# Kernel tuning notes

Measured on AMD Instinct MI355X. Metric: run time of the kernel, lower is better.

The kernel has to match this reference:

```python
import jax, jax.numpy as jnp
from jax import lax
import numpy as np

K = 31      # avg_pool2d kernel_size
PAD = 15    # avg_pool2d padding
EPS = 1.0
GAMMA = 5.0


def _box_avg(x):
    # Separable 31x31 box filter, stride 1, zero padding 15,
    # count_include_pad=True (PyTorch default) -> always divide by K*K.
    s = lax.reduce_window(x, 0.0, lax.add, (1, 1, K, 1), (1, 1, 1, 1),
                          [(0, 0), (0, 0), (PAD, PAD), (0, 0)])
    s = lax.reduce_window(s, 0.0, lax.add, (1, 1, 1, K), (1, 1, 1, 1),
                          [(0, 0), (0, 0), (0, 0), (PAD, PAD)])
    return s / (K * K)


def setup_inputs() -> dict:
    key = jax.random.key(0)
    k1, k2 = jax.random.split(key)
    shape = (64, 1, 512, 512)  # [B, C, H, W]
    inp = jax.random.uniform(k1, shape, dtype=jnp.float32)
    tgt = jax.random.uniform(k2, shape, dtype=jnp.float32)
    return {"input": inp, "target": tgt}


def reference(input, target):
    weight = 1.0 + GAMMA * jnp.abs(_box_avg(target) - target)
    intersection = jnp.sum(input * target * weight)
    denom = jnp.sum(input * weight) + jnp.sum(target * weight)
    dice = (2.0 * intersection + EPS) / (denom + EPS)
    return 1.0 - dice
```

## Files before the change

kernel.cpp:

```cpp
#include <hip/hip_runtime.h>


#define BATCH 64
#define H     512
#define W     512
#define PADR  15
#define NSEG  32
#define RB    (H / NSEG)
#define NBLK  (BATCH * NSEG)

__global__ __launch_bounds__(64) void fused_kernel(const float* __restrict__ tgt,
                                                   const float* __restrict__ inp,
                                                   float4* __restrict__ partials) {
    const int lane = threadIdx.x;
    const int blk  = blockIdx.x;
    const int band = blk & (NSEG - 1);
    const int b    = blk >> 5;
    const int r0   = band * RB;
    const int col0 = lane * 8;
    const float* timg = tgt + (size_t)b * H * W;
    const float* iimg = inp + (size_t)b * H * W;

    float vr[8];
    #pragma unroll
    for (int k = 0; k < 8; ++k) vr[k] = 0.f;
    #pragma unroll
    for (int j = -PADR; j <= PADR; ++j) {
        const int r = r0 + j;
        if (r >= 0 && r < H) {
            const float4 a = *(const float4*)(timg + (size_t)r * W + col0);
            const float4 c = *(const float4*)(timg + (size_t)r * W + col0 + 4);
            vr[0] += a.x; vr[1] += a.y; vr[2] += a.z; vr[3] += a.w;
            vr[4] += c.x; vr[5] += c.y; vr[6] += c.z; vr[7] += c.w;
        }
    }

    float validf[40];
    #pragma unroll
    for (int m = 0; m < 40; ++m) {
        const int c = col0 - 16 + m;
        validf[m] = (c >= 0 && c < W) ? 1.f : 0.f;
    }

    const float inv = 1.0f / 961.0f;
    float aI = 0.f, aA = 0.f, aB = 0.f;

    for (int h = r0; h < r0 + RB; ++h) {
        float wd[40];
        #pragma unroll
        for (int k = 0; k < 8; ++k) {
            wd[k]      = __shfl_up(vr[k], 2, 64);
            wd[k + 8]  = __shfl_up(vr[k], 1, 64);
            wd[k + 16] = vr[k];
            wd[k + 24] = __shfl_down(vr[k], 1, 64);
            wd[k + 32] = __shfl_down(vr[k], 2, 64);
        }
        #pragma unroll
        for (int m = 0; m < 40; ++m) wd[m] *= validf[m];

        float run = 0.f;
        #pragma unroll
        for (int m = 1; m <= 31; ++m) run += wd[m];

        const float4 t0 = *(const float4*)(timg + (size_t)h * W + col0);
        const float4 t1 = *(const float4*)(timg + (size_t)h * W + col0 + 4);
        const float4 i0 = *(const float4*)(iimg + (size_t)h * W + col0);
        const float4 i1 = *(const float4*)(iimg + (size_t)h * W + col0 + 4);
        const float tv[8] = {t0.x, t0.y, t0.z, t0.w, t1.x, t1.y, t1.z, t1.w};
        const float iv[8] = {i0.x, i0.y, i0.z, i0.w, i1.x, i1.y, i1.z, i1.w};

        #pragma unroll
        for (int j = 0; j < 8; ++j) {
            const float wgt = 1.0f + 5.0f * fabsf(run * inv - tv[j]);
            aI += iv[j] * tv[j] * wgt;
            aA += iv[j] * wgt;
            aB += tv[j] * wgt;
            run += wd[j + 32] - wd[j + 1];
        }

        const int add = h + PADR + 1;
        const int sub = h - PADR;
        if (add < H) {
            const float4 a = *(const float4*)(timg + (size_t)add * W + col0);
            const float4 c = *(const float4*)(timg + (size_t)add * W + col0 + 4);
            vr[0] += a.x; vr[1] += a.y; vr[2] += a.z; vr[3] += a.w;
            vr[4] += c.x; vr[5] += c.y; vr[6] += c.z; vr[7] += c.w;
        }
        if (sub >= 0) {
            const float4 a = *(const float4*)(timg + (size_t)sub * W + col0);
            const float4 c = *(const float4*)(timg + (size_t)sub * W + col0 + 4);
            vr[0] -= a.x; vr[1] -= a.y; vr[2] -= a.z; vr[3] -= a.w;
            vr[4] -= c.x; vr[5] -= c.y; vr[6] -= c.z; vr[7] -= c.w;
        }
    }

    #pragma unroll
    for (int off = 32; off > 0; off >>= 1) {
        aI += __shfl_down(aI, off, 64);
        aA += __shfl_down(aA, off, 64);
        aB += __shfl_down(aB, off, 64);
    }
    if (lane == 0) {
        float4 o; o.x = aI; o.y = aA; o.z = aB; o.w = 0.f;
        partials[blk] = o;
    }
}

__global__ __launch_bounds__(1024) void reduce_kernel(const float4* __restrict__ partials,
                                                      float* __restrict__ out) {
    const int tid = threadIdx.x;
    float aI = 0.f, aA = 0.f, aB = 0.f;
    #pragma unroll
    for (int i = tid; i < NBLK; i += 1024) {
        const float4 v = partials[i];
        aI += v.x; aA += v.y; aB += v.z;
    }
    #pragma unroll
    for (int off = 32; off > 0; off >>= 1) {
        aI += __shfl_down(aI, off, 64);
        aA += __shfl_down(aA, off, 64);
        aB += __shfl_down(aB, off, 64);
    }
    __shared__ float s[3][16];
    const int wv = tid >> 6, ln = tid & 63;
    if (ln == 0) { s[0][wv] = aI; s[1][wv] = aA; s[2][wv] = aB; }
    __syncthreads();
    if (tid == 0) {
        float I = 0.f, A = 0.f, Bv = 0.f;
        #pragma unroll
        for (int k = 0; k < 16; ++k) { I += s[0][k]; A += s[1][k]; Bv += s[2][k]; }
        out[0] = 1.0f - (2.0f * I + 1.0f) / (A + Bv + 1.0f);
    }
}

extern "C" void kernel_launch(void* const* d_in, const int* in_sizes, int n_in,
                              void* d_out, int out_size, void* d_ws, size_t ws_size,
                              hipStream_t stream) {
    const float* inp = (const float*)d_in[0];
    const float* tgt = (const float*)d_in[1];
    float* out = (float*)d_out;

    float4* partials = (float4*)d_ws;

    fused_kernel<<<NBLK, 64, 0, stream>>>(tgt, inp, partials);
    reduce_kernel<<<1, 1024, 0, stream>>>(partials, out);
}
```

Measured before the change: 169.0 us.

## Compute horizontal box window via prefix sums and fewer shuffles; pack 4 waves per block

Replaces the 40-element shuffled window plus sliding running sum with per-lane prefix/suffix sums over the 8 column sums. Each output's 31-wide window is built from the lane's own total, its neighbours' totals, and shuffled partial sums from lanes two away. This cuts shuffles from 32 to 16 per row and removes the 40-element masking, which lowers register and VALU pressure. Row bands are halved (NSEG 64) for more parallelism, at the cost of more redundant vertical-window warm-up reads. Four waves are packed into each 256-thread block, with a shared-memory combine before the partial write.

```diff
diff --git a/kernel.cpp b/kernel.cpp
--- a/kernel.cpp
+++ b/kernel.cpp
@@ -5,21 +5,29 @@
 #define H     512
 #define W     512
 #define PADR  15
-#define NSEG  32
+#define NSEG  64
 #define RB    (H / NSEG)
-#define NBLK  (BATCH * NSEG)
+#define NWAVE (BATCH * NSEG)
+#define NBLK  (NWAVE / 4)
 
-__global__ __launch_bounds__(64) void fused_kernel(const float* __restrict__ tgt,
-                                                   const float* __restrict__ inp,
-                                                   float4* __restrict__ partials) {
-    const int lane = threadIdx.x;
-    const int blk  = blockIdx.x;
-    const int band = blk & (NSEG - 1);
-    const int b    = blk >> 5;
+__global__ __launch_bounds__(256) void fused_kernel(const float* __restrict__ tgt,
+                                                    const float* __restrict__ inp,
+                                                    float4* __restrict__ partials) {
+    const int tid  = threadIdx.x;
+    const int lane = tid & 63;
+    const int wv   = tid >> 6;
+    const int g    = blockIdx.x * 4 + wv;
+    const int band = g & (NSEG - 1);
+    const int b    = g >> 6;
     const int r0   = band * RB;
     const int col0 = lane * 8;
     const float* timg = tgt + (size_t)b * H * W;
     const float* iimg = inp + (size_t)b * H * W;
+
+    const float mL1 = (lane >= 1) ? 1.f : 0.f;
+    const float mR1 = (lane <= 62) ? 1.f : 0.f;
+    const float mL2 = (lane >= 2) ? 1.f : 0.f;
+    const float mR2 = (lane <= 61) ? 1.f : 0.f;
 
     float vr[8];
     #pragma unroll
@@ -35,32 +43,48 @@
         }
     }
 
-    float validf[40];
-    #pragma unroll
-    for (int m = 0; m < 40; ++m) {
-        const int c = col0 - 16 + m;
-        validf[m] = (c >= 0 && c < W) ? 1.f : 0.f;
-    }
-
     const float inv = 1.0f / 961.0f;
     float aI = 0.f, aA = 0.f, aB = 0.f;
 
     for (int h = r0; h < r0 + RB; ++h) {
-        float wd[40];
-        #pragma unroll
-        for (int k = 0; k < 8; ++k) {
-            wd[k]      = __shfl_up(vr[k], 2, 64);
-            wd[k + 8]  = __shfl_up(vr[k], 1, 64);
-            wd[k + 16] = vr[k];
-            wd[k + 24] = __shfl_down(vr[k], 1, 64);
-            wd[k + 32] = __shfl_down(vr[k], 2, 64);
-        }
-        #pragma unroll
-        for (int m = 0; m < 40; ++m) wd[m] *= validf[m];
+        const float p1 = vr[0];
+        const float p2 = p1 + vr[1];
+        const float p3 = p2 + vr[2];
+        const float p4 = p3 + vr[3];
+        const float p5 = p4 + vr[4];
+        const float p6 = p5 + vr[5];
+        const float p7 = p6 + vr[6];
+        const float s  = p7 + vr[7];
+        const float f1 = s - p1, f2 = s - p2, f3 = s - p3, f4 = s - p4;
+        const float f5 = s - p5, f6 = s - p6, f7 = s - p7;
 
-        float run = 0.f;
-        #pragma unroll
-        for (int m = 1; m <= 31; ++m) run += wd[m];
+        const float sL1 = __shfl_up(s, 1, 64);
+        const float sR1 = __shfl_down(s, 1, 64);
+        const float g1 = __shfl_up(f1, 2, 64);
+        const float g2 = __shfl_up(f2, 2, 64);
+        const float g3 = __shfl_up(f3, 2, 64);
+        const float g4 = __shfl_up(f4, 2, 64);
+        const float g5 = __shfl_up(f5, 2, 64);
+        const float g6 = __shfl_up(f6, 2, 64);
+        const float g7 = __shfl_up(f7, 2, 64);
+        const float q1 = __shfl_down(p1, 2, 64);
+        const float q2 = __shfl_down(p2, 2, 64);
+        const float q3 = __shfl_down(p3, 2, 64);
+        const float q4 = __shfl_down(p4, 2, 64);
+        const float q5 = __shfl_down(p5, 2, 64);
+        const float q6 = __shfl_down(p6, 2, 64);
+        const float q7 = __shfl_down(p7, 2, 64);
+
+        const float S3 = fmaf(mL1, sL1, fmaf(mR1, sR1, s));
+        float win[8];
+        win[0] = fmaf(mL2, g1, S3);
+        win[1] = fmaf(mL2, g2, fmaf(mR2, q1, S3));
+        win[2] = fmaf(mL2, g3, fmaf(mR2, q2, S3));
+        win[3] = fmaf(mL2, g4, fmaf(mR2, q3, S3));
+        win[4] = fmaf(mL2, g5, fmaf(mR2, q4, S3));
+        win[5] = fmaf(mL2, g6, fmaf(mR2, q5, S3));
+        win[6] = fmaf(mL2, g7, fmaf(mR2, q6, S3));
+        win[7] = fmaf(mR2, q7, S3);
 
         const float4 t0 = *(const float4*)(timg + (size_t)h * W + col0);
         const float4 t1 = *(const float4*)(timg + (size_t)h * W + col0 + 4);
@@ -71,11 +95,10 @@
 
         #pragma unroll
         for (int j = 0; j < 8; ++j) {
-            const float wgt = 1.0f + 5.0f * fabsf(run * inv - tv[j]);
+            const float wgt = fmaf(5.0f, fabsf(fmaf(win[j], inv, -tv[j])), 1.0f);
             aI += iv[j] * tv[j] * wgt;
             aA += iv[j] * wgt;
             aB += tv[j] * wgt;
-            run += wd[j + 32] - wd[j + 1];
         }
 
         const int add = h + PADR + 1;
@@ -100,9 +123,16 @@
         aA += __shfl_down(aA, off, 64);
         aB += __shfl_down(aB, off, 64);
     }
-    if (lane == 0) {
-        float4 o; o.x = aI; o.y = aA; o.z = aB; o.w = 0.f;
-        partials[blk] = o;
+    __shared__ float part[3][4];
+    if (lane == 0) { part[0][wv] = aI; part[1][wv] = aA; part[2][wv] = aB; }
+    __syncthreads();
+    if (tid == 0) {
+        float4 o;
+        o.x = part[0][0] + part[0][1] + part[0][2] + part[0][3];
+        o.y = part[1][0] + part[1][1] + part[1][2] + part[1][3];
+        o.z = part[2][0] + part[2][1] + part[2][2] + part[2][3];
+        o.w = 0.f;
+        partials[blockIdx.x] = o;
     }
 }
 
@@ -110,7 +140,6 @@
                                                       float* __restrict__ out) {
     const int tid = threadIdx.x;
     float aI = 0.f, aA = 0.f, aB = 0.f;
-    #pragma unroll
     for (int i = tid; i < NBLK; i += 1024) {
         const float4 v = partials[i];
         aI += v.x; aA += v.y; aB += v.z;
@@ -122,8 +151,8 @@
         aB += __shfl_down(aB, off, 64);
     }
     __shared__ float s[3][16];
-    const int wv = tid >> 6, ln = tid & 63;
-    if (ln == 0) { s[0][wv] = aI; s[1][wv] = aA; s[2][wv] = aB; }
+    const int wvx = tid >> 6, ln = tid & 63;
+    if (ln == 0) { s[0][wvx] = aI; s[1][wvx] = aA; s[2][wvx] = aB; }
     __syncthreads();
     if (tid == 0) {
         float I = 0.f, A = 0.f, Bv = 0.f;
@@ -142,6 +171,6 @@
 
     float4* partials = (float4*)d_ws;
 
-    fused_kernel<<<NBLK, 64, 0, stream>>>(tgt, inp, partials);
+    fused_kernel<<<NBLK, 256, 0, stream>>>(tgt, inp, partials);
     reduce_kernel<<<1, 1024, 0, stream>>>(partials, out);
 }
```

Result: slower. 175.0 us (+3.6%).
